# Kernel tuning notes

Hardware: AMD Instinct MI355X
Metric: run time of the kernel (lower is better)

Reference implementation:

```python
import jax, jax.numpy as jnp
import numpy as np

D = 40       # d_model
SL = 10      # sequenceLength
AN = 268     # actionNum
B = 8192     # batch


def relu6(x):
    return jnp.clip(x, 0.0, 6.0)


def setup_inputs() -> dict:
    key = jax.random.key(0)
    ks = jax.random.split(key, 16)
    s = 1.0 / np.sqrt(D)
    X = jax.random.randint(ks[0], (B, SL, 4), 0, AN)
    t1 = jax.random.randint(ks[1], (B, SL - 1), 0, 7)
    t2 = jax.random.randint(ks[2], (B, SL - 1), 0, 8)
    # per-step Linear(1, D): weight [D,1] -> store as [SL-1, D]; kaiming-uniform bound 1/sqrt(1)=1
    Ew = jax.random.uniform(ks[3], (SL - 1, D), minval=-1.0, maxval=1.0)
    Eb = jax.random.uniform(ks[4], (SL - 1, D), minval=-1.0, maxval=1.0)
    Qw = jax.random.uniform(ks[5], (SL - 1, D, D), minval=-s, maxval=s)
    Qb = jax.random.uniform(ks[6], (SL - 1, D), minval=-s, maxval=s)
    Lw = jax.random.uniform(ks[7], (SL - 1, D * D, D), minval=-s, maxval=s)
    Lb = jax.random.uniform(ks[8], (SL - 1, D * D), minval=-s, maxval=s)
    Mw = jax.random.uniform(ks[9], (SL - 1, D, D), minval=-s, maxval=s)
    Mb = jax.random.uniform(ks[10], (SL - 1, D), minval=-s, maxval=s)
    Tw = jax.random.uniform(ks[11], (AN, D), minval=-s, maxval=s)
    Tb = jax.random.uniform(ks[12], (AN,), minval=-s, maxval=s)
    emb = jax.random.normal(ks[13], (AN, D))
    return dict(X=X, t1=t1, t2=t2, Ew=Ew, Eb=Eb, Qw=Qw, Qb=Qb, Lw=Lw, Lb=Lb,
                Mw=Mw, Mb=Mb, Tw=Tw, Tb=Tb, emb=emb)


def reference(X, t1, t2, Ew, Eb, Qw, Qb, Lw, Lb, Mw, Mb, Tw, Tb, emb):
    b = X.shape[0]
    t = (t1 * 8 + t2).astype(jnp.float32)          # [B, SL-1]
    ae = emb[X[:, :SL - 1, 3]]                     # [B, SL-1, D]

    def step(carry, xs):
        h0, p0 = carry
        ew, eb, qw, qb, lw, lb, mw, mb, ti, ei = xs
        # E(t_i) + Q(p0), both [B, D]
        p1 = relu6(ti[:, None] * ew[None, :] + eb + p0 @ qw.T + qb)
        # hypernetwork-generated per-sample matrix [B, D, D]
        jt = relu6(p1 @ lw.T + lb).reshape(b, D, D)
        tt = jnp.einsum('bd,bde->be', h0, jt)
        h1 = relu6(ei @ mw.T + mb + tt)
        return (h1, p1), None

    xs = (Ew, Eb, Qw, Qb, Lw, Lb, Mw, Mb, t.T, jnp.swapaxes(ae, 0, 1))
    init = (jnp.zeros((b, D), jnp.float32), jnp.zeros((b, D), jnp.float32))
    (h0, _), _ = jax.lax.scan(step, init, xs)
    return h0 @ Tw.T + Tb                          # [B, AN]
```

## Files before the change

kernel.cpp:

```cpp
#include <hip/hip_runtime.h>

#define DD 40
#define SLM1 9
#define ANUM 268
#define MB 32

typedef __attribute__((ext_vector_type(8))) short short8;
typedef __attribute__((ext_vector_type(4))) float f32x4;
typedef __attribute__((ext_vector_type(16))) float f32x16;

#define WS_LWF ((size_t)0)
#define WS_LWT ((size_t)552960)
#define WS_QW  ((size_t)691200)
#define WS_MW  ((size_t)718848)
#define WS_TW  ((size_t)746496)

__device__ __forceinline__ unsigned short f2bf(float f){
  unsigned int u = __float_as_uint(f);
  u += 0x7FFFu + ((u >> 16) & 1u);
  return (unsigned short)(u >> 16);
}
__device__ __forceinline__ float relu6f(float v){
  return fminf(fmaxf(v, 0.0f), 6.0f);
}

__device__ __forceinline__ f32x16 mfma3(short8 a0, short8 a1, short8 a2,
                                        short8 b0, short8 b1, short8 b2){
  f32x16 c = {0,0,0,0,0,0,0,0,0,0,0,0,0,0,0,0};
  c = __builtin_amdgcn_mfma_f32_32x32x16_bf16(a0, b0, c, 0, 0, 0);
  c = __builtin_amdgcn_mfma_f32_32x32x16_bf16(a1, b1, c, 0, 0, 0);
  c = __builtin_amdgcn_mfma_f32_32x32x16_bf16(a2, b2, c, 0, 0, 0);
  return c;
}

__global__ __launch_bounds__(256)
void prep_frags(const float* __restrict__ Qw, const float* __restrict__ Lw,
                const float* __restrict__ Mw, const float* __restrict__ Tw,
                const float* __restrict__ Ew, const float* __restrict__ Eb,
                const float* __restrict__ Qb, const float* __restrict__ Lb,
                const float* __restrict__ Mb, const float* __restrict__ Tb,
                unsigned short* __restrict__ ws)
{
  const int bid = blockIdx.x, tid = threadIdx.x;
  if (bid < 360){
    int s = bid / 40, d = bid - s*40;
    unsigned short* dst = ws + WS_LWF + (size_t)bid*1536;
    const float* W = Lw + (size_t)s*64000;
    const float* bv = Lb + (size_t)s*1600;
    for (int i = tid; i < 1536; i += 256){
      int kf = i >> 9, q = i & 511, l = q >> 3, j = q & 7;
      int k = kf*16 + ((l >> 5) << 3) + j;
      int e = l & 31;
      int n = d*DD + e;
      float v = 0.f;
      if (k < DD) v = W[n*DD + k];
      else if (k == DD) v = bv[n];
      dst[i] = f2bf(v);
    }
  } else if (bid < 450){
    int t = bid - 360;
    int s = t / 10, tt = t - s*10;
    unsigned short* dst = ws + WS_LWT + (size_t)t*1536;
    const float* W = Lw + (size_t)s*64000;
    const float* bv = Lb + (size_t)s*1600;
    for (int i = tid; i < 1536; i += 256){
      int kf = i >> 9, q = i & 511, l = q >> 3, j = q & 7;
      int k = kf*16 + ((l >> 5) << 3) + j;
      int c = l & 31;
      int d = 4*tt + (c >> 3);
      int e = 32 + (c & 7);
      int n = d*DD + e;
      float v = 0.f;
      if (k < DD) v = W[n*DD + k];
      else if (k == DD) v = bv[n];
      dst[i] = f2bf(v);
    }
  } else if (bid < 459){
    int s = bid - 450;
    unsigned short* dst = ws + WS_QW + (size_t)s*3072;
    const float* W = Qw + (size_t)s*1600;
    for (int i = tid; i < 3072; i += 256){
      int et = i / 1536, r = i - et*1536;
      int kf = r >> 9, q = r & 511, l = q >> 3, j = q & 7;
      int k = kf*16 + ((l >> 5) << 3) + j;
      int jc = et*32 + (l & 31);
      float v = 0.f;
      if (jc < DD){
        if (k < DD) v = W[jc*DD + k];
        else if (k == DD) v = Eb[s*DD + jc] + Qb[s*DD + jc];
        else if (k == DD+1) v = Ew[s*DD + jc];
      }
      dst[i] = f2bf(v);
    }
  } else if (bid < 468){
    int s = bid - 459;
    unsigned short* dst = ws + WS_MW + (size_t)s*3072;
    const float* W = Mw + (size_t)s*1600;
    for (int i = tid; i < 3072; i += 256){
      int et = i / 1536, r = i - et*1536;
      int kf = r >> 9, q = r & 511, l = q >> 3, j = q & 7;
      int k = kf*16 + ((l >> 5) << 3) + j;
      int e = et*32 + (l & 31);
      float v = 0.f;
      if (e < DD){
        if (k < DD) v = W[e*DD + k];
        else if (k == DD) v = Mb[s*DD + e];
      }
      dst[i] = f2bf(v);
    }
  } else {
    int t = bid - 468;
    unsigned short* dst = ws + WS_TW + (size_t)t*1536;
    for (int i = tid; i < 1536; i += 256){
      int kf = i >> 9, q = i & 511, l = q >> 3, j = q & 7;
      int k = kf*16 + ((l >> 5) << 3) + j;
      int a = t*32 + (l & 31);
      float v = 0.f;
      if (a < ANUM){
        if (k < DD) v = Tw[(size_t)a*DD + k];
        else if (k == DD) v = Tb[a];
      }
      dst[i] = f2bf(v);
    }
  }
}

__global__ __launch_bounds__(512)
void star_main(const int* __restrict__ X,
               const int* __restrict__ T1,
               const int* __restrict__ T2,
               const float* __restrict__ emb,
               const unsigned short* __restrict__ ws,
               float* __restrict__ out)
{
  __shared__ __align__(16) unsigned short pbuf[2][3072];
  __shared__ __align__(16) unsigned short aebf[2][3072];
  __shared__ __align__(16) float hT[2][DD*36];
  __shared__ __align__(16) float red[8][MB*DD];
  __shared__ int   aeidx[SLM1][MB];
  __shared__ float tvtab[SLM1][MB];

  const int tid = threadIdx.x;
  const int w = __builtin_amdgcn_readfirstlane(tid >> 6);
  const int l = tid & 63;
  const int col = l & 31, half = l >> 5;
  const int row0 = blockIdx.x * MB;

  {
    unsigned int* p = (unsigned int*)&pbuf[0][0];
    for (int i = tid; i < 3072; i += 512) p[i] = 0u;
    unsigned int* a = (unsigned int*)&aebf[0][0];
    for (int i = tid; i < 3072; i += 512) a[i] = 0u;
    float* rr = &red[0][0];
    for (int i = tid; i < 8*MB*DD; i += 512) rr[i] = 0.f;
  }
  if (tid < MB*SLM1){
    int m = tid / SLM1, s = tid - m*SLM1;
    int r = row0 + m;
    aeidx[s][m] = X[(size_t)r*40 + s*4 + 3];
    tvtab[s][m] = (float)(T1[r*SLM1 + s]*8 + T2[r*SLM1 + s]);
  }
  __syncthreads();
  if (tid < MB){
    int off = 2*1024 + (tid + 32)*8;
    pbuf[0][off] = 0x3F80; pbuf[1][off] = 0x3F80;
    aebf[0][off] = 0x3F80; aebf[1][off] = 0x3F80;
    pbuf[0][off+1] = f2bf(tvtab[0][tid]);
    pbuf[1][off+1] = f2bf(tvtab[1][tid]);
  }
  if (tid < 320){
    int m = tid / 10, q4 = tid - m*10;
    float4 v4 = *(const float4*)(emb + (size_t)aeidx[0][m]*DD + q4*4);
    #pragma unroll
    for (int c2 = 0; c2 < 4; ++c2){
      int k = q4*4 + c2, kf = k >> 4, kk = k & 15;
      aebf[0][kf*1024 + (m + ((kk >> 3) << 5))*8 + (kk & 7)] = f2bf(((const float*)&v4)[c2]);
    }
  }
  __syncthreads();
  if (w < 2){
    short8 a0 = ((const short8*)&pbuf[0][0])[l];
    short8 a1 = ((const short8*)&pbuf[0][1024])[l];
    short8 a2 = ((const short8*)&pbuf[0][2048])[l];
    const unsigned short* qwb = ws + WS_QW + w*1536;
    f32x16 c = mfma3(a0, a1, a2, ((const short8*)qwb)[l],
                     ((const short8*)(qwb+512))[l], ((const short8*)(qwb+1024))[l]);
    int j = w*32 + col;
    if (j < DD){
      int kf = j >> 4, kk = j & 15;
      #pragma unroll
      for (int r = 0; r < 16; ++r){
        int m = (r & 3) + ((r >> 2) << 3) + (half << 2);
        pbuf[1][kf*1024 + (m + ((kk >> 3) << 5))*8 + (kk & 7)] = f2bf(relu6f(c[r]));
      }
    }
  }
  __syncthreads();

  for (int s = 0; s < SLM1; ++s){
    const int pcur = (s + 1) & 1;
    const int hrd  = s & 1;

    float4 gv; int gm = 0, gq = 0;
    const bool dog = (s < 8) && (tid < 320);
    if (dog){
      gm = tid / 10; gq = tid - gm*10;
      gv = *(const float4*)(emb + (size_t)aeidx[s+1][gm]*DD + gq*4);
    }
    if (s > 0){
      short8 pa0 = ((const short8*)&pbuf[pcur][0])[l];
      short8 pa1 = ((const short8*)&pbuf[pcur][1024])[l];
      short8 pa2 = ((const short8*)&pbuf[pcur][2048])[l];
      const float* hbase = &hT[hrd][half << 2];

      f32x16 tt = {0,0,0,0,0,0,0,0,0,0,0,0,0,0,0,0};
      {
        const unsigned short* lwf = ws + WS_LWF + (size_t)(s*40)*1536;
        const unsigned short* f0 = lwf + (size_t)w*1536;
        short8 b00 = ((const short8*)f0)[l];
        short8 b01 = ((const short8*)(f0 + 512))[l];
        short8 b02 = ((const short8*)(f0 + 1024))[l];
        const unsigned short* f1 = lwf + (size_t)(8 + w)*1536;
        short8 b10 = ((const short8*)f1)[l];
        short8 b11 = ((const short8*)(f1 + 512))[l];
        short8 b12 = ((const short8*)(f1 + 1024))[l];
        #pragma unroll
        for (int i = 0; i < 5; ++i){
          short8 nb0, nb1, nb2;
          if (i < 3){
            const unsigned short* nf = lwf + (size_t)((i+2)*8 + w)*1536;
            nb0 = ((const short8*)nf)[l];
            nb1 = ((const short8*)(nf + 512))[l];
            nb2 = ((const short8*)(nf + 1024))[l];
          }
          f32x16 c = mfma3(pa0, pa1, pa2, b00, b01, b02);
          const float* hb = hbase + (i*8 + w)*36;
          #pragma unroll
          for (int g = 0; g < 4; ++g){
            f32x4 hg = *(const f32x4*)(hb + g*8);
            #pragma unroll
            for (int q = 0; q < 4; ++q)
              tt[g*4+q] = fmaf(hg[q], relu6f(c[g*4+q]), tt[g*4+q]);
          }
          b00 = b10; b01 = b11; b02 = b12;
          if (i < 3){ b10 = nb0; b11 = nb1; b12 = nb2; }
        }
      }
      #pragma unroll
      for (int r = 0; r < 16; ++r){
        int m = (r & 3) + ((r >> 2) << 3) + (half << 2);
        red[w][m*DD + col] = tt[r];
      }

      const unsigned short* lwt = ws + WS_LWT + (size_t)(s*10)*1536;
      f32x16 tacc = {0,0,0,0,0,0,0,0,0,0,0,0,0,0,0,0};
      for (int tti = w; tti < 10; tti += 8){
        const unsigned short* ft = lwt + (size_t)tti*1536;
        short8 t0 = ((const short8*)ft)[l];
        short8 t1 = ((const short8*)(ft + 512))[l];
        short8 t2 = ((const short8*)(ft + 1024))[l];
        f32x16 c = mfma3(pa0, pa1, pa2, t0, t1, t2);
        int dt = 4*tti + (col >> 3);
        const float* hb = &hT[hrd][dt*36 + (half << 2)];
        #pragma unroll
        for (int g = 0; g < 4; ++g){
          f32x4 hg = *(const f32x4*)(hb + g*8);
          #pragma unroll
          for (int q = 0; q < 4; ++q){
            float val = hg[q]*relu6f(c[g*4+q]);
            val += __shfl_xor(val, 8);
            val += __shfl_xor(val, 16);
            tacc[g*4+q] += val;
          }
        }
      }
      if (col < 8){
        #pragma unroll
        for (int r = 0; r < 16; ++r){
          int m = (r & 3) + ((r >> 2) << 3) + (half << 2);
          red[w][m*DD + 32 + col] = tacc[r];
        }
      }
    }
    if (dog){
      unsigned short* dst = &aebf[(s+1) & 1][0];
      #pragma unroll
      for (int c2 = 0; c2 < 4; ++c2){
        int k = gq*4 + c2, kf = k >> 4, kk = k & 15;
        dst[kf*1024 + (gm + ((kk >> 3) << 5))*8 + (kk & 7)] = f2bf(((const float*)&gv)[c2]);
      }
    }
    if (s <= 6 && tid < MB)
      pbuf[s & 1][2*1024 + (tid + 32)*8 + 1] = f2bf(tvtab[s+2][tid]);
    __syncthreads();

    if (w < 2){
      short8 a0 = ((const short8*)&aebf[s & 1][0])[l];
      short8 a1 = ((const short8*)&aebf[s & 1][1024])[l];
      short8 a2 = ((const short8*)&aebf[s & 1][2048])[l];
      const unsigned short* mwb = ws + WS_MW + (size_t)s*3072 + w*1536;
      int e = w*32 + col;
      f32x16 c = {0,0,0,0,0,0,0,0,0,0,0,0,0,0,0,0};
      if (e < DD){
        #pragma unroll
        for (int r = 0; r < 16; ++r){
          int m = (r & 3) + ((r >> 2) << 3) + (half << 2);
          float acc = red[0][m*DD + e];
          #pragma unroll
          for (int dp = 1; dp < 8; ++dp) acc += red[dp][m*DD + e];
          c[r] = acc;
        }
      }
      c = __builtin_amdgcn_mfma_f32_32x32x16_bf16(a0, ((const short8*)mwb)[l], c, 0, 0, 0);
      c = __builtin_amdgcn_mfma_f32_32x32x16_bf16(a1, ((const short8*)(mwb+512))[l], c, 0, 0, 0);
      c = __builtin_amdgcn_mfma_f32_32x32x16_bf16(a2, ((const short8*)(mwb+1024))[l], c, 0, 0, 0);
      if (e < DD){
        int kf = e >> 4, kk = e & 15;
        #pragma unroll
        for (int r = 0; r < 16; ++r){
          int m = (r & 3) + ((r >> 2) << 3) + (half << 2);
          float v = relu6f(c[r]);
          hT[(s+1) & 1][e*36 + m] = v;
          if (s == SLM1-1)
            aebf[1][kf*1024 + (m + ((kk >> 3) << 5))*8 + (kk & 7)] = f2bf(v);
        }
      }
    } else if (w < 4 && s < 8){
      const int et = w - 2;
      short8 a0 = ((const short8*)&pbuf[pcur][0])[l];
      short8 a1 = ((const short8*)&pbuf[pcur][1024])[l];
      short8 a2 = ((const short8*)&pbuf[pcur][2048])[l];
      const unsigned short* qwb = ws + WS_QW + (size_t)(s+1)*3072 + et*1536;
      f32x16 c = mfma3(a0, a1, a2, ((const short8*)qwb)[l],
                       ((const short8*)(qwb+512))[l], ((const short8*)(qwb+1024))[l]);
      int j = et*32 + col;
      if (j < DD){
        int kf = j >> 4, kk = j & 15;
        #pragma unroll
        for (int r = 0; r < 16; ++r){
          int m = (r & 3) + ((r >> 2) << 3) + (half << 2);
          pbuf[s & 1][kf*1024 + (m + ((kk >> 3) << 5))*8 + (kk & 7)] = f2bf(relu6f(c[r]));
        }
      }
    }
    __syncthreads();
  }

  for (int t = w; t < 9; t += 8){
    short8 a0 = ((const short8*)&aebf[1][0])[l];
    short8 a1 = ((const short8*)&aebf[1][1024])[l];
    short8 a2 = ((const short8*)&aebf[1][2048])[l];
    const unsigned short* twb = ws + WS_TW + (size_t)t*1536;
    f32x16 c = mfma3(a0, a1, a2, ((const short8*)twb)[l],
                     ((const short8*)(twb+512))[l], ((const short8*)(twb+1024))[l]);
    int a = t*32 + col;
    if (a < ANUM){
      #pragma unroll
      for (int r = 0; r < 16; ++r){
        int m = (r & 3) + ((r >> 2) << 3) + (half << 2);
        out[(size_t)(row0 + m)*ANUM + a] = c[r];
      }
    }
  }
}

extern "C" void kernel_launch(void* const* d_in, const int* in_sizes, int n_in,
                              void* d_out, int out_size, void* d_ws, size_t ws_size,
                              hipStream_t stream) {
  const int*   X  = (const int*)  d_in[0];
  const int*   T1 = (const int*)  d_in[1];
  const int*   T2 = (const int*)  d_in[2];
  const float* Ew = (const float*)d_in[3];
  const float* Eb = (const float*)d_in[4];
  const float* Qw = (const float*)d_in[5];
  const float* Qb = (const float*)d_in[6];
  const float* Lw = (const float*)d_in[7];
  const float* Lb = (const float*)d_in[8];
  const float* Mw = (const float*)d_in[9];
  const float* Mb = (const float*)d_in[10];
  const float* Tw = (const float*)d_in[11];
  const float* Tb = (const float*)d_in[12];
  const float* em = (const float*)d_in[13];
  unsigned short* ws = (unsigned short*)d_ws;
  float* out = (float*)d_out;

  prep_frags<<<dim3(477), dim3(256), 0, stream>>>(Qw, Lw, Mw, Tw, Ew, Eb, Qb,
                                                  Lb, Mb, Tb, ws);
  star_main<<<dim3(8192 / MB), dim3(512), 0, stream>>>(X, T1, T2, em, ws, out);
}
```

Baseline: 58.11 us.

## Prefetch next-step hypernet weights and move Q projection into first phase

```diff
diff --git a/kernel.cpp b/kernel.cpp
--- a/kernel.cpp
+++ b/kernel.cpp
@@ -197,6 +197,8 @@
   }
   __syncthreads();
 
+  short8 q00, q01, q02, q10, q11, q12;
+
   for (int s = 0; s < SLM1; ++s){
     const int pcur = (s + 1) & 1;
     const int hrd  = s & 1;
@@ -207,23 +209,17 @@
       gm = tid / 10; gq = tid - gm*10;
       gv = *(const float4*)(emb + (size_t)aeidx[s+1][gm]*DD + gq*4);
     }
+    short8 pa0 = ((const short8*)&pbuf[pcur][0])[l];
+    short8 pa1 = ((const short8*)&pbuf[pcur][1024])[l];
+    short8 pa2 = ((const short8*)&pbuf[pcur][2048])[l];
     if (s > 0){
-      short8 pa0 = ((const short8*)&pbuf[pcur][0])[l];
-      short8 pa1 = ((const short8*)&pbuf[pcur][1024])[l];
-      short8 pa2 = ((const short8*)&pbuf[pcur][2048])[l];
       const float* hbase = &hT[hrd][half << 2];
 
       f32x16 tt = {0,0,0,0,0,0,0,0,0,0,0,0,0,0,0,0};
       {
         const unsigned short* lwf = ws + WS_LWF + (size_t)(s*40)*1536;
-        const unsigned short* f0 = lwf + (size_t)w*1536;
-        short8 b00 = ((const short8*)f0)[l];
-        short8 b01 = ((const short8*)(f0 + 512))[l];
-        short8 b02 = ((const short8*)(f0 + 1024))[l];
-        const unsigned short* f1 = lwf + (size_t)(8 + w)*1536;
-        short8 b10 = ((const short8*)f1)[l];
-        short8 b11 = ((const short8*)(f1 + 512))[l];
-        short8 b12 = ((const short8*)(f1 + 1024))[l];
+        short8 b00 = q00, b01 = q01, b02 = q02;
+        short8 b10 = q10, b11 = q11, b12 = q12;
         #pragma unroll
         for (int i = 0; i < 5; ++i){
           short8 nb0, nb1, nb2;
@@ -233,14 +229,18 @@
             nb1 = ((const short8*)(nf + 512))[l];
             nb2 = ((const short8*)(nf + 1024))[l];
           }
+          const float* hb = hbase + (i*8 + w)*36;
+          f32x4 h0 = *(const f32x4*)(hb);
+          f32x4 h1 = *(const f32x4*)(hb + 8);
+          f32x4 h2 = *(const f32x4*)(hb + 16);
+          f32x4 h3 = *(const f32x4*)(hb + 24);
           f32x16 c = mfma3(pa0, pa1, pa2, b00, b01, b02);
-          const float* hb = hbase + (i*8 + w)*36;
           #pragma unroll
-          for (int g = 0; g < 4; ++g){
-            f32x4 hg = *(const f32x4*)(hb + g*8);
-            #pragma unroll
-            for (int q = 0; q < 4; ++q)
-              tt[g*4+q] = fmaf(hg[q], relu6f(c[g*4+q]), tt[g*4+q]);
+          for (int q = 0; q < 4; ++q){
+            tt[q]    = fmaf(h0[q], relu6f(c[q]),    tt[q]);
+            tt[4+q]  = fmaf(h1[q], relu6f(c[4+q]),  tt[4+q]);
+            tt[8+q]  = fmaf(h2[q], relu6f(c[8+q]),  tt[8+q]);
+            tt[12+q] = fmaf(h3[q], relu6f(c[12+q]), tt[12+q]);
           }
           b00 = b10; b01 = b11; b02 = b12;
           if (i < 3){ b10 = nb0; b11 = nb1; b12 = nb2; }
@@ -251,10 +251,24 @@
         int m = (r & 3) + ((r >> 2) << 3) + (half << 2);
         red[w][m*DD + col] = tt[r];
       }
-
+    }
+
+    if (s < 8){
+      const unsigned short* nl = ws + WS_LWF + (size_t)((s+1)*40)*1536;
+      const unsigned short* n0 = nl + (size_t)w*1536;
+      q00 = ((const short8*)n0)[l];
+      q01 = ((const short8*)(n0 + 512))[l];
+      q02 = ((const short8*)(n0 + 1024))[l];
+      const unsigned short* n1 = nl + (size_t)(8 + w)*1536;
+      q10 = ((const short8*)n1)[l];
+      q11 = ((const short8*)(n1 + 512))[l];
+      q12 = ((const short8*)(n1 + 1024))[l];
+    }
+
+    if (s > 0 && w < 6){
       const unsigned short* lwt = ws + WS_LWT + (size_t)(s*10)*1536;
       f32x16 tacc = {0,0,0,0,0,0,0,0,0,0,0,0,0,0,0,0};
-      for (int tti = w; tti < 10; tti += 8){
+      for (int tti = w; tti < 10; tti += 6){
         const unsigned short* ft = lwt + (size_t)tti*1536;
         short8 t0 = ((const short8*)ft)[l];
         short8 t1 = ((const short8*)(ft + 512))[l];
@@ -281,6 +295,20 @@
           red[w][m*DD + 32 + col] = tacc[r];
         }
       }
+    } else if (w >= 6 && s < 8){
+      const int et = w - 6;
+      const unsigned short* qwb = ws + WS_QW + (size_t)(s+1)*3072 + (size_t)et*1536;
+      f32x16 c = mfma3(pa0, pa1, pa2, ((const short8*)qwb)[l],
+                       ((const short8*)(qwb+512))[l], ((const short8*)(qwb+1024))[l]);
+      int j = et*32 + col;
+      if (j < DD){
+        int kf = j >> 4, kk = j & 15;
+        #pragma unroll
+        for (int r = 0; r < 16; ++r){
+          int m = (r & 3) + ((r >> 2) << 3) + (half << 2);
+          pbuf[s & 1][kf*1024 + (m + ((kk >> 3) << 5))*8 + (kk & 7)] = f2bf(relu6f(c[r]));
+        }
+      }
     }
     if (dog){
       unsigned short* dst = &aebf[(s+1) & 1][0];
@@ -323,23 +351,6 @@
           hT[(s+1) & 1][e*36 + m] = v;
           if (s == SLM1-1)
             aebf[1][kf*1024 + (m + ((kk >> 3) << 5))*8 + (kk & 7)] = f2bf(v);
-        }
-      }
-    } else if (w < 4 && s < 8){
-      const int et = w - 2;
-      short8 a0 = ((const short8*)&pbuf[pcur][0])[l];
-      short8 a1 = ((const short8*)&pbuf[pcur][1024])[l];
-      short8 a2 = ((const short8*)&pbuf[pcur][2048])[l];
-      const unsigned short* qwb = ws + WS_QW + (size_t)(s+1)*3072 + et*1536;
-      f32x16 c = mfma3(a0, a1, a2, ((const short8*)qwb)[l],
-                       ((const short8*)(qwb+512))[l], ((const short8*)(qwb+1024))[l]);
-      int j = et*32 + col;
-      if (j < DD){
-        int kf = j >> 4, kk = j & 15;
-        #pragma unroll
-        for (int r = 0; r < 16; ++r){
-          int m = (r & 3) + ((r >> 2) << 3) + (half << 2);
-          pbuf[s & 1][kf*1024 + (m + ((kk >> 3) << 5))*8 + (kk & 7)] = f2bf(relu6f(c[r]));
         }
       }
     }
```

Result: no change. 57.32 us (-1.4%).
